# Optimization experiments

Hardware: AMD Instinct MI355X
Metric: run time of the kernel (lower is better)

## Reference

```python
import jax, jax.numpy as jnp
import numpy as np

N_NODES = 20000
N_RELS = 64
RP = 8
EMB = 64
N_CLASSES = 16
NT = 250000      # unique (subject, object) pairs
N_TRIPLES = 500000


def setup_inputs() -> dict:
    rng = np.random.default_rng(0)
    # sample candidate (s, o) pairs, dedupe (mirrors torch.unique(pairs, dim=0)),
    # keep exactly NT unique pairs
    cand = rng.integers(0, N_NODES, size=(NT + 60000, 2))
    pairs = np.unique(cand, axis=0)
    assert pairs.shape[0] >= NT
    pairs = pairs[:NT]
    # each triple maps to a unique-pair row and a relation column;
    # relation_matrix is the coalesced sparse_coo (nt, num_rels) densified
    row = rng.integers(0, NT, size=N_TRIPLES)
    rel = rng.integers(0, N_RELS, size=N_TRIPLES)
    relation_matrix = np.zeros((NT, N_RELS), dtype=np.float32)
    np.add.at(relation_matrix, (row, rel), 1.0)
    # hindices / vindices exactly as in __init__ (note the literal o*r / s*r):
    s, o = pairs[:, 0].astype(np.int64), pairs[:, 1].astype(np.int64)
    rm = np.arange(RP, dtype=np.int64)[:, None]
    hrow = np.tile(s, RP)                      # (RP*NT,) row in [0, N)
    hcol = (o[None, :] * rm).reshape(-1)       # (RP*NT,) col in [0, N*RP)
    vrow = (s[None, :] * rm).reshape(-1)       # (RP*NT,) row in [0, N*RP)
    vcol = np.tile(o, RP)                      # (RP*NT,) col in [0, N)

    key = jax.random.key(0)
    ks = jax.random.split(key, 6)

    def xavier(k, shape, fan_in, fan_out):
        gain = np.float32(np.sqrt(2.0))  # calculate_gain('relu')
        bound = gain * np.float32(np.sqrt(6.0 / (fan_in + fan_out)))
        return jax.random.uniform(k, shape, jnp.float32, -bound, bound)

    lb = np.float32(1.0 / np.sqrt(N_RELS))  # nn.Linear default init bound
    return {
        "relation_matrix": jnp.asarray(relation_matrix),
        "hrow": jnp.asarray(hrow), "hcol": jnp.asarray(hcol),
        "vrow": jnp.asarray(vrow), "vcol": jnp.asarray(vcol),
        "W_l1": jax.random.uniform(ks[0], (N_RELS, RP), jnp.float32, -lb, lb),
        "b_l1": jax.random.uniform(ks[1], (RP,), jnp.float32, -lb, lb),
        "W_l2": jax.random.uniform(ks[2], (N_RELS, RP), jnp.float32, -lb, lb),
        "b_l2": jax.random.uniform(ks[3], (RP,), jnp.float32, -lb, lb),
        "weights1": xavier(ks[4], (RP, N_NODES, EMB), N_NODES * EMB, RP * EMB),
        "weights2": xavier(ks[5], (RP, EMB, N_CLASSES), EMB * N_CLASSES, RP * N_CLASSES),
        "bias1": jnp.zeros((EMB,), jnp.float32),
        "bias2": jnp.zeros((N_CLASSES,), jnp.float32),
    }


def reference(relation_matrix, hrow, hcol, vrow, vcol,
              W_l1, b_l1, W_l2, b_l2, weights1, weights2, bias1, bias2):
    n, rp, e = N_NODES, RP, EMB
    nrp = n * rp
    # ---- hop 1: latent coefficients (to_latent1, ldepth=0 => single Linear)
    l1 = relation_matrix @ W_l1 + b_l1              # (NT, RP)
    l1 = l1.T.reshape(-1)                           # (RP*NT,) r-major, matches h/v index order
    # sum_sparse(hindices, l1, (n, n*rp), row=False): per-edge column-sum normalization
    colsum = jax.ops.segment_sum(l1, hcol, num_segments=nrp)
    l1 = l1 / colsum[hcol]
    # spmm over hindices: out[hrow] += l1 * weights1.view(n*rp, e)[hcol]
    Wflat = weights1.reshape(nrp, e)                # (N*RP, EMB)
    h = jax.ops.segment_sum(l1[:, None] * Wflat[hcol], hrow, num_segments=n)
    h = jax.nn.relu(h + bias1)                      # (N, EMB)
    # ---- hop 2
    l2 = jax.nn.softmax(relation_matrix @ W_l2 + b_l2, axis=1)  # (NT, RP)
    l2 = jax.nn.relu(l2.T.reshape(-1))              # (RP*NT,)
    # sum_sparse(vindices, l2, (n*rp, n), row=True): per-edge row-sum normalization
    rowsum = jax.ops.segment_sum(l2, vrow, num_segments=nrp)
    l2 = l2 / jnp.maximum(rowsum[vrow], 1e-6)
    # spmm over vindices: out[vrow] += l2 * h[vcol]
    h2 = jax.ops.segment_sum(l2[:, None] * h[vcol], vrow, num_segments=nrp)
    h2 = h2.reshape(rp, n, e)                       # (RP, N, EMB)
    logits = jnp.einsum('rhc,rnh->nc', weights2, h2) + bias2  # (N, C)
    return logits
```

## Files before the change

### kernel.cpp

```cpp
#include <hip/hip_runtime.h>
#include <hip/hip_fp16.h>

#define NT      250000
#define NN      20000
#define RP      8
#define EMB     64
#define NCLS    16
#define NRELS   64
#define REDB    64
#define KMAX    140000
#define GEMVB   977
#define RPB     79
#define HIB     977
#define OIB     1250

__global__ __launch_bounds__(256) void k_gemv(
    const float* __restrict__ rm,
    const float* __restrict__ W1, const float* __restrict__ b1,
    const float* __restrict__ W2, const float* __restrict__ b2,
    float* __restrict__ l1, float* __restrict__ l2,
    const int* __restrict__ hrow, int* __restrict__ rowptr,
    const int* __restrict__ vcol, int* __restrict__ cnt,
    float* __restrict__ out, const float* __restrict__ bias2)
{
    __shared__ float tile[256 * 20];
    int bid = blockIdx.x;
    if (bid >= GEMVB) {
        int b = bid - GEMVB;
        if (b < RPB) {
            int i = b * 256 + threadIdx.x;
            if (i > NN) return;
            int lo = 0, hi = NT;
            while (lo < hi) { int mid = (lo + hi) >> 1; if (hrow[mid] < i) lo = mid + 1; else hi = mid; }
            rowptr[i] = lo;
        } else if (b < RPB + HIB) {
            int p = (b - RPB) * 256 + threadIdx.x;
            if (p < NT) atomicAdd(&cnt[vcol[p]], 1);
        } else {
            int i = (b - RPB - HIB) * 256 + threadIdx.x;
            if (i < NN * NCLS) out[i] = bias2[i & (NCLS - 1)];
        }
        return;
    }
    int t = threadIdx.x;
    int base = bid * 256;
    float a1[8], a2[8];
#pragma unroll
    for (int r = 0; r < 8; ++r) { a1[r] = b1[r]; a2[r] = b2[r]; }

#pragma unroll 1
    for (int kc = 0; kc < 4; ++kc) {
        __syncthreads();
#pragma unroll
        for (int q = 0; q < 4; ++q) {
            int i = q * 256 + t;
            int pl = i >> 2, j4 = i & 3;
            int p = base + pl;
            float4 v = make_float4(0.f, 0.f, 0.f, 0.f);
            if (p < NT) v = reinterpret_cast<const float4*>(rm)[(size_t)p * 16 + kc * 4 + j4];
            *reinterpret_cast<float4*>(&tile[pl * 20 + j4 * 4]) = v;
        }
        __syncthreads();
        float xr[16];
#pragma unroll
        for (int j4 = 0; j4 < 4; ++j4) {
            float4 v = *reinterpret_cast<const float4*>(&tile[t * 20 + j4 * 4]);
            xr[j4 * 4 + 0] = v.x; xr[j4 * 4 + 1] = v.y;
            xr[j4 * 4 + 2] = v.z; xr[j4 * 4 + 3] = v.w;
        }
#pragma unroll
        for (int kk = 0; kk < 16; ++kk) {
            float x = xr[kk];
            int k = kc * 16 + kk;
#pragma unroll
            for (int r = 0; r < 8; ++r) {
                a1[r] = fmaf(x, W1[k * 8 + r], a1[r]);
                a2[r] = fmaf(x, W2[k * 8 + r], a2[r]);
            }
        }
    }
    int p = base + t;
    if (p >= NT) return;
    float mx = a2[0];
#pragma unroll
    for (int r = 1; r < 8; ++r) mx = fmaxf(mx, a2[r]);
    float sm = 0.f;
#pragma unroll
    for (int r = 0; r < 8; ++r) { a2[r] = __expf(a2[r] - mx); sm += a2[r]; }
    float inv = 1.0f / sm;
#pragma unroll
    for (int r = 0; r < 8; ++r) a2[r] *= inv;
    float4* o1 = reinterpret_cast<float4*>(l1 + (size_t)p * 8);
    float4* o2 = reinterpret_cast<float4*>(l2 + (size_t)p * 8);
    o1[0] = make_float4(a1[0], a1[1], a1[2], a1[3]);
    o1[1] = make_float4(a1[4], a1[5], a1[6], a1[7]);
    o2[0] = make_float4(a2[0], a2[1], a2[2], a2[3]);
    o2[1] = make_float4(a2[4], a2[5], a2[6], a2[7]);
}

__global__ __launch_bounds__(1024) void k_scan(
    const int* __restrict__ cnt, int* __restrict__ cstart, int* __restrict__ cnt2)
{
    __shared__ int part[1024];
    int t = threadIdx.x;
    int base = t * 20;
    int local[20];
    int s = 0;
#pragma unroll
    for (int i = 0; i < 20; ++i) {
        int idx = base + i;
        int c = (idx < NN) ? cnt[idx] : 0;
        local[i] = s;
        s += c;
    }
    part[t] = s;
    __syncthreads();
    for (int off = 1; off < 1024; off <<= 1) {
        int v = (t >= off) ? part[t - off] : 0;
        __syncthreads();
        part[t] += v;
        __syncthreads();
    }
    int ebase = t ? part[t - 1] : 0;
#pragma unroll
    for (int i = 0; i < 20; ++i) {
        int idx = base + i;
        if (idx < NN) { cstart[idx] = ebase + local[i]; cnt2[idx] = ebase + local[i]; }
    }
    if (t == 1023) cstart[NN] = part[1023];
}

__global__ __launch_bounds__(256) void k_pos(
    const int* __restrict__ vcol, int* __restrict__ cnt2, int* __restrict__ cscidx)
{
    int p = blockIdx.x * blockDim.x + threadIdx.x;
    if (p >= NT) return;
    int o = vcol[p];
    int slot = atomicAdd(&cnt2[o], 1);
    cscidx[slot] = p;
}

__global__ __launch_bounds__(256) void k_colsum(
    const float* __restrict__ l1, const int* __restrict__ cstart,
    const int* __restrict__ cscidx, float* __restrict__ colsum)
{
    int bid = blockIdx.x;
    if (bid < NN / 4) {
        int o = bid * 4 + (threadIdx.x >> 6);
        int lane = threadIdx.x & 63;
        int qb = cstart[o], qe = cstart[o + 1];
        if (qb == qe) return;
        int j = lane >> 3, r = lane & 7;
        float sum = 0.f;
        for (int q0 = qb; q0 < qe; q0 += 8) {
            int q = q0 + j;
            if (q < qe) sum += l1[(size_t)cscidx[q] * 8 + r];
        }
        sum += __shfl_xor(sum, 8, 64);
        sum += __shfl_xor(sum, 16, 64);
        sum += __shfl_xor(sum, 32, 64);
        if (lane >= 1 && lane < 8) atomicAdd(&colsum[o * lane], sum);
    } else {
        int b2 = bid - NN / 4;
        float s = 0.f;
        for (int i = b2 * 256 + threadIdx.x; i < NT; i += REDB * 256) s += l1[(size_t)i * 8];
        __shared__ float red[256];
        red[threadIdx.x] = s;
        __syncthreads();
        for (int off = 128; off > 0; off >>= 1) {
            if (threadIdx.x < off) red[threadIdx.x] += red[threadIdx.x + off];
            __syncthreads();
        }
        if (threadIdx.x == 0) atomicAdd(&colsum[0], red[0]);
    }
}

__global__ __launch_bounds__(256) void k_contrib(
    const float* __restrict__ l1, const float* __restrict__ colsum,
    const int* __restrict__ cstart, const int* __restrict__ cscidx,
    const float* __restrict__ w1, __half* __restrict__ contrib)
{
    int o = (int)((blockIdx.x * blockDim.x + threadIdx.x) >> 6);
    int lane = threadIdx.x & 63;
    if (o >= NN) return;
    int qb = cstart[o], qe = cstart[o + 1];
    if (qb == qe) return;
    float y[8];
    y[0] = w1[lane] / colsum[0];
#pragma unroll
    for (int r = 1; r < 8; ++r) {
        int seg = o * r;
        y[r] = w1[(size_t)seg * EMB + lane] / colsum[seg];
    }
    int q = qb;
    for (; q + 3 < qe; q += 4) {
        int p0 = cscidx[q], p1 = cscidx[q + 1], p2 = cscidx[q + 2], p3 = cscidx[q + 3];
        const float4* a4 = reinterpret_cast<const float4*>(l1 + (size_t)p0 * 8);
        const float4* b4 = reinterpret_cast<const float4*>(l1 + (size_t)p1 * 8);
        const float4* c4 = reinterpret_cast<const float4*>(l1 + (size_t)p2 * 8);
        const float4* d4 = reinterpret_cast<const float4*>(l1 + (size_t)p3 * 8);
        float4 A = a4[0], B = a4[1], C = b4[0], D = b4[1];
        float4 E = c4[0], F = c4[1], G = d4[0], H = d4[1];
        float v0 = A.x * y[0];
        v0 = fmaf(A.y, y[1], v0); v0 = fmaf(A.z, y[2], v0); v0 = fmaf(A.w, y[3], v0);
        v0 = fmaf(B.x, y[4], v0); v0 = fmaf(B.y, y[5], v0);
        v0 = fmaf(B.z, y[6], v0); v0 = fmaf(B.w, y[7], v0);
        float v1 = C.x * y[0];
        v1 = fmaf(C.y, y[1], v1); v1 = fmaf(C.z, y[2], v1); v1 = fmaf(C.w, y[3], v1);
        v1 = fmaf(D.x, y[4], v1); v1 = fmaf(D.y, y[5], v1);
        v1 = fmaf(D.z, y[6], v1); v1 = fmaf(D.w, y[7], v1);
        float v2 = E.x * y[0];
        v2 = fmaf(E.y, y[1], v2); v2 = fmaf(E.z, y[2], v2); v2 = fmaf(E.w, y[3], v2);
        v2 = fmaf(F.x, y[4], v2); v2 = fmaf(F.y, y[5], v2);
        v2 = fmaf(F.z, y[6], v2); v2 = fmaf(F.w, y[7], v2);
        float v3 = G.x * y[0];
        v3 = fmaf(G.y, y[1], v3); v3 = fmaf(G.z, y[2], v3); v3 = fmaf(G.w, y[3], v3);
        v3 = fmaf(H.x, y[4], v3); v3 = fmaf(H.y, y[5], v3);
        v3 = fmaf(H.z, y[6], v3); v3 = fmaf(H.w, y[7], v3);
        contrib[(size_t)p0 * EMB + lane] = __float2half(v0);
        contrib[(size_t)p1 * EMB + lane] = __float2half(v1);
        contrib[(size_t)p2 * EMB + lane] = __float2half(v2);
        contrib[(size_t)p3 * EMB + lane] = __float2half(v3);
    }
    for (; q < qe; ++q) {
        int p0 = cscidx[q];
        const float4* a4 = reinterpret_cast<const float4*>(l1 + (size_t)p0 * 8);
        float4 A = a4[0], B = a4[1];
        float v0 = A.x * y[0];
        v0 = fmaf(A.y, y[1], v0); v0 = fmaf(A.z, y[2], v0); v0 = fmaf(A.w, y[3], v0);
        v0 = fmaf(B.x, y[4], v0); v0 = fmaf(B.y, y[5], v0);
        v0 = fmaf(B.z, y[6], v0); v0 = fmaf(B.w, y[7], v0);
        contrib[(size_t)p0 * EMB + lane] = __float2half(v0);
    }
}

__global__ __launch_bounds__(256) void k_h(
    const __half* __restrict__ contrib, const float* __restrict__ l2,
    const int* __restrict__ rowptr, const float* __restrict__ bias1,
    __half* __restrict__ h, float* __restrict__ rowsum, float* __restrict__ rs0part)
{
    int s = (int)((blockIdx.x * blockDim.x + threadIdx.x) >> 6);
    int lane = threadIdx.x & 63;
    if (s >= NN) return;
    int pb = rowptr[s], pe = rowptr[s + 1];
    float acc = 0.f;
    for (int p = pb; p < pe; ++p)
        acc += __half2float(contrib[(size_t)p * EMB + lane]);
    h[(size_t)s * EMB + lane] = __float2half(fmaxf(acc + bias1[lane], 0.f));

    float psum = 0.f;
    for (int p0 = pb + (lane >> 3); p0 < pe; p0 += 8)
        psum += l2[(size_t)p0 * 8 + (lane & 7)];
    psum += __shfl_xor(psum, 8, 64);
    psum += __shfl_xor(psum, 16, 64);
    psum += __shfl_xor(psum, 32, 64);
    if (s == 0) {
        float tt = psum;
        tt += __shfl_xor(tt, 1, 64);
        tt += __shfl_xor(tt, 2, 64);
        tt += __shfl_xor(tt, 4, 64);
        if (lane == 0) rs0part[0] = tt;
    } else {
        if (lane == 0) rs0part[s] = psum;
        else if (lane < 8) atomicAdd(&rowsum[s * lane], psum);
    }
}

__global__ __launch_bounds__(256) void k_l2out(
    const float* __restrict__ l2, const int* __restrict__ rowptr,
    const int* __restrict__ vcol, const __half* __restrict__ h,
    const float* __restrict__ rowsum, const float* __restrict__ w2,
    float* __restrict__ out, float* __restrict__ Abuf0)
{
    int s = (int)((blockIdx.x * blockDim.x + threadIdx.x) >> 6);
    int lane = threadIdx.x & 63;
    if (s >= NN) return;
    int pb = rowptr[s], pe = rowptr[s + 1];
    float sc[8];
#pragma unroll
    for (int rr = 1; rr < 8; ++rr)
        sc[rr] = (s > 0) ? (1.0f / fmaxf(rowsum[s * rr], 1e-6f)) : 0.f;
    float acc[8];
#pragma unroll
    for (int r = 0; r < 8; ++r) acc[r] = 0.f;
    int p = pb;
    for (; p + 3 < pe; p += 4) {
        int o0 = vcol[p], o1 = vcol[p + 1], o2 = vcol[p + 2], o3 = vcol[p + 3];
        float hv0 = __half2float(h[(size_t)o0 * EMB + lane]);
        float hv1 = __half2float(h[(size_t)o1 * EMB + lane]);
        float hv2 = __half2float(h[(size_t)o2 * EMB + lane]);
        float hv3 = __half2float(h[(size_t)o3 * EMB + lane]);
        const float4* q4 = reinterpret_cast<const float4*>(l2 + (size_t)p * 8);
        float4 A = q4[0], B = q4[1], C = q4[2], D = q4[3];
        float4 E = q4[4], F = q4[5], G = q4[6], H = q4[7];
        acc[0] = fmaf(A.x, hv0, fmaf(C.x, hv1, fmaf(E.x, hv2, fmaf(G.x, hv3, acc[0]))));
        acc[1] = fmaf(A.y, hv0, fmaf(C.y, hv1, fmaf(E.y, hv2, fmaf(G.y, hv3, acc[1]))));
        acc[2] = fmaf(A.z, hv0, fmaf(C.z, hv1, fmaf(E.z, hv2, fmaf(G.z, hv3, acc[2]))));
        acc[3] = fmaf(A.w, hv0, fmaf(C.w, hv1, fmaf(E.w, hv2, fmaf(G.w, hv3, acc[3]))));
        acc[4] = fmaf(B.x, hv0, fmaf(D.x, hv1, fmaf(F.x, hv2, fmaf(H.x, hv3, acc[4]))));
        acc[5] = fmaf(B.y, hv0, fmaf(D.y, hv1, fmaf(F.y, hv2, fmaf(H.y, hv3, acc[5]))));
        acc[6] = fmaf(B.z, hv0, fmaf(D.z, hv1, fmaf(F.z, hv2, fmaf(H.z, hv3, acc[6]))));
        acc[7] = fmaf(B.w, hv0, fmaf(D.w, hv1, fmaf(F.w, hv2, fmaf(H.w, hv3, acc[7]))));
    }
    for (; p < pe; ++p) {
        int o0 = vcol[p];
        float hv0 = __half2float(h[(size_t)o0 * EMB + lane]);
        const float4* q4 = reinterpret_cast<const float4*>(l2 + (size_t)p * 8);
        float4 A = q4[0], B = q4[1];
        acc[0] = fmaf(A.x, hv0, acc[0]); acc[1] = fmaf(A.y, hv0, acc[1]);
        acc[2] = fmaf(A.z, hv0, acc[2]); acc[3] = fmaf(A.w, hv0, acc[3]);
        acc[4] = fmaf(B.x, hv0, acc[4]); acc[5] = fmaf(B.y, hv0, acc[5]);
        acc[6] = fmaf(B.z, hv0, acc[6]); acc[7] = fmaf(B.w, hv0, acc[7]);
    }
    if (s == 0) {
        float a = acc[0] + acc[1] + acc[2] + acc[3] +
                  acc[4] + acc[5] + acc[6] + acc[7];
        Abuf0[lane] = a;
        return;
    }
    Abuf0[(size_t)s * EMB + lane] = acc[0];
    if (pb == pe) return;
    int hq = lane >> 4, c = lane & 15;
#pragma unroll
    for (int rr = 1; rr < 8; ++rr) {
        int k = s * rr;
        int rp = k / NN;
        int n  = k - rp * NN;
        float v = 0.f;
#pragma unroll
        for (int hh = 0; hh < 16; ++hh) {
            float av = __shfl(acc[rr], hq * 16 + hh, 64);
            v = fmaf(av, w2[((rp * EMB) + (hq * 16 + hh)) * NCLS + c], v);
        }
        v += __shfl_xor(v, 16, 64);
        v += __shfl_xor(v, 32, 64);
        if (lane < 16) atomicAdd(&out[(size_t)n * NCLS + lane], v * sc[rr]);
    }
}

__global__ __launch_bounds__(256) void k_redA(
    const float* __restrict__ Abuf0, const float* __restrict__ rs0part,
    const float* __restrict__ w2, float* __restrict__ out)
{
    __shared__ float red[256];
    __shared__ float part[64];
    __shared__ float irs0s;
    float sv = 0.f;
    for (int i = threadIdx.x; i < NN; i += 256) sv += rs0part[i];
    red[threadIdx.x] = sv;
    __syncthreads();
    for (int off = 128; off > 0; off >>= 1) {
        if (threadIdx.x < off) red[threadIdx.x] += red[threadIdx.x + off];
        __syncthreads();
    }
    if (threadIdx.x == 0) irs0s = 1.0f / fmaxf(red[0], 1e-6f);
    __syncthreads();
    float irs0 = irs0s;
    int lane = threadIdx.x & 63, w = threadIdx.x >> 6;
    float sum = 0.f;
    for (int ss = blockIdx.x + 64 * w; ss < NN; ss += 256)
        sum += Abuf0[(size_t)ss * EMB + lane];
    red[threadIdx.x] = sum;
    __syncthreads();
    if (threadIdx.x < 64) {
        part[threadIdx.x] = red[threadIdx.x] + red[threadIdx.x + 64] +
                            red[threadIdx.x + 128] + red[threadIdx.x + 192];
    }
    __syncthreads();
    if (threadIdx.x < 64) {
        int hq = threadIdx.x >> 4, c = threadIdx.x & 15;
        float v = 0.f;
#pragma unroll
        for (int hh = 0; hh < 16; ++hh) {
            int hd = hq * 16 + hh;
            v = fmaf(part[hd], w2[hd * NCLS + c], v);
        }
        v += __shfl_xor(v, 16, 64);
        v += __shfl_xor(v, 32, 64);
        if (threadIdx.x < 16) atomicAdd(&out[c], v * irs0);
    }
}

extern "C" void kernel_launch(void* const* d_in, const int* in_sizes, int n_in,
                              void* d_out, int out_size, void* d_ws, size_t ws_size,
                              hipStream_t stream)
{
    const float* rm    = (const float*)d_in[0];
    const int*   hrow  = (const int*)d_in[1];
    const int*   vcol  = (const int*)d_in[4];
    const float* W1    = (const float*)d_in[5];
    const float* b1    = (const float*)d_in[6];
    const float* W2    = (const float*)d_in[7];
    const float* b2    = (const float*)d_in[8];
    const float* w1    = (const float*)d_in[9];
    const float* w2    = (const float*)d_in[10];
    const float* bias1 = (const float*)d_in[11];
    const float* bias2 = (const float*)d_in[12];
    float* out = (float*)d_out;

    float* ws = (float*)d_ws;
    float*  l1      = ws;
    float*  l2      = ws + 2000000;
    int*    rowptr  = (int*)(ws + 4000000);
    float*  colsum  = ws + 4100000;
    float*  rowsum  = ws + 4260000;
    __half* h       = (__half*)(ws + 4400000);
    int*    cnt     = (int*)(ws + 5040000);
    int*    cstart  = cnt + 20000;
    int*    cnt2    = cstart + 20001;
    int*    cscidx  = cnt2 + 20000;
    __half* contrib = (__half*)(ws + 5600000);
    float*  Abuf0   = ws;
    float*  rs0part = ws + 1280000;

    hipMemsetAsync(colsum, 0, (size_t)300000 * sizeof(float), stream);
    hipMemsetAsync(cnt, 0, (size_t)20000 * sizeof(int), stream);

    k_gemv   <<<GEMVB + RPB + HIB + OIB, 256, 0, stream>>>(rm, W1, b1, W2, b2, l1, l2,
                                                           hrow, rowptr, vcol, cnt, out, bias2);
    k_scan   <<<1, 1024, 0, stream>>>(cnt, cstart, cnt2);
    k_pos    <<<(NT + 255) / 256, 256, 0, stream>>>(vcol, cnt2, cscidx);
    k_colsum <<<NN / 4 + REDB, 256, 0, stream>>>(l1, cstart, cscidx, colsum);
    k_contrib<<<(NN * 64) / 256, 256, 0, stream>>>(l1, colsum, cstart, cscidx, w1, contrib);
    k_h      <<<(NN * 64) / 256, 256, 0, stream>>>(contrib, l2, rowptr, bias1, h, rowsum, rs0part);
    k_l2out  <<<(NN * 64) / 256, 256, 0, stream>>>(l2, rowptr, vcol, h, rowsum, w2, out, Abuf0);
    k_redA   <<<64, 256, 0, stream>>>(Abuf0, rs0part, w2, out);
}
```

Baseline: 233.2 us.

## Scatter hop-1 contributions via float atomics instead of half staging buffer

The per-pair contribution kernel now atomically adds each fp32 value straight into a per-subject accumulator h_acc. Previously it wrote a 250000x64 half buffer that k_h then re-read and summed per row. This removes a large intermediate write and read pass but adds 16M global float atomics, which may contend on popular subjects and make summation order nondeterministic. The workspace is rearranged so a single memset zeroes cnt, colsum, rowsum and h_acc. A reciprocal division is also swapped for the hardware rcp intrinsic.

After: 255.4 us. 1.09x slower.

```diff
diff --git a/kernel.cpp b/kernel.cpp
--- a/kernel.cpp
+++ b/kernel.cpp
@@ -175,10 +175,11 @@
     }
 }
 
-__global__ __launch_bounds__(256) void k_contrib(
+__global__ __launch_bounds__(256) void k_hacc(
     const float* __restrict__ l1, const float* __restrict__ colsum,
     const int* __restrict__ cstart, const int* __restrict__ cscidx,
-    const float* __restrict__ w1, __half* __restrict__ contrib)
+    const int* __restrict__ hrow, const float* __restrict__ w1,
+    float* __restrict__ h_acc)
 {
     int o = (int)((blockIdx.x * blockDim.x + threadIdx.x) >> 6);
     int lane = threadIdx.x & 63;
@@ -195,6 +196,7 @@
     int q = qb;
     for (; q + 3 < qe; q += 4) {
         int p0 = cscidx[q], p1 = cscidx[q + 1], p2 = cscidx[q + 2], p3 = cscidx[q + 3];
+        int s0 = hrow[p0], s1 = hrow[p1], s2 = hrow[p2], s3 = hrow[p3];
         const float4* a4 = reinterpret_cast<const float4*>(l1 + (size_t)p0 * 8);
         const float4* b4 = reinterpret_cast<const float4*>(l1 + (size_t)p1 * 8);
         const float4* c4 = reinterpret_cast<const float4*>(l1 + (size_t)p2 * 8);
@@ -217,25 +219,26 @@
         v3 = fmaf(G.y, y[1], v3); v3 = fmaf(G.z, y[2], v3); v3 = fmaf(G.w, y[3], v3);
         v3 = fmaf(H.x, y[4], v3); v3 = fmaf(H.y, y[5], v3);
         v3 = fmaf(H.z, y[6], v3); v3 = fmaf(H.w, y[7], v3);
-        contrib[(size_t)p0 * EMB + lane] = __float2half(v0);
-        contrib[(size_t)p1 * EMB + lane] = __float2half(v1);
-        contrib[(size_t)p2 * EMB + lane] = __float2half(v2);
-        contrib[(size_t)p3 * EMB + lane] = __float2half(v3);
+        atomicAdd(&h_acc[(size_t)s0 * EMB + lane], v0);
+        atomicAdd(&h_acc[(size_t)s1 * EMB + lane], v1);
+        atomicAdd(&h_acc[(size_t)s2 * EMB + lane], v2);
+        atomicAdd(&h_acc[(size_t)s3 * EMB + lane], v3);
     }
     for (; q < qe; ++q) {
         int p0 = cscidx[q];
+        int s0 = hrow[p0];
         const float4* a4 = reinterpret_cast<const float4*>(l1 + (size_t)p0 * 8);
         float4 A = a4[0], B = a4[1];
         float v0 = A.x * y[0];
         v0 = fmaf(A.y, y[1], v0); v0 = fmaf(A.z, y[2], v0); v0 = fmaf(A.w, y[3], v0);
         v0 = fmaf(B.x, y[4], v0); v0 = fmaf(B.y, y[5], v0);
         v0 = fmaf(B.z, y[6], v0); v0 = fmaf(B.w, y[7], v0);
-        contrib[(size_t)p0 * EMB + lane] = __float2half(v0);
+        atomicAdd(&h_acc[(size_t)s0 * EMB + lane], v0);
     }
 }
 
 __global__ __launch_bounds__(256) void k_h(
-    const __half* __restrict__ contrib, const float* __restrict__ l2,
+    const float* __restrict__ h_acc, const float* __restrict__ l2,
     const int* __restrict__ rowptr, const float* __restrict__ bias1,
     __half* __restrict__ h, float* __restrict__ rowsum, float* __restrict__ rs0part)
 {
@@ -243,9 +246,7 @@
     int lane = threadIdx.x & 63;
     if (s >= NN) return;
     int pb = rowptr[s], pe = rowptr[s + 1];
-    float acc = 0.f;
-    for (int p = pb; p < pe; ++p)
-        acc += __half2float(contrib[(size_t)p * EMB + lane]);
+    float acc = h_acc[(size_t)s * EMB + lane];
     h[(size_t)s * EMB + lane] = __float2half(fmaxf(acc + bias1[lane], 0.f));
 
     float psum = 0.f;
@@ -279,7 +280,7 @@
     float sc[8];
 #pragma unroll
     for (int rr = 1; rr < 8; ++rr)
-        sc[rr] = (s > 0) ? (1.0f / fmaxf(rowsum[s * rr], 1e-6f)) : 0.f;
+        sc[rr] = (s > 0) ? __builtin_amdgcn_rcpf(fmaxf(rowsum[s * rr], 1e-6f)) : 0.f;
     float acc[8];
 #pragma unroll
     for (int r = 0; r < 8; ++r) acc[r] = 0.f;
@@ -402,27 +403,26 @@
     float*  l1      = ws;
     float*  l2      = ws + 2000000;
     int*    rowptr  = (int*)(ws + 4000000);
+    int*    cnt     = (int*)(ws + 4030000);
     float*  colsum  = ws + 4100000;
     float*  rowsum  = ws + 4260000;
-    __half* h       = (__half*)(ws + 4400000);
-    int*    cnt     = (int*)(ws + 5040000);
-    int*    cstart  = cnt + 20000;
+    float*  h_acc   = ws + 4400000;
+    __half* h       = (__half*)(ws + 5680000);
+    int*    cstart  = (int*)(ws + 6400000);
     int*    cnt2    = cstart + 20001;
     int*    cscidx  = cnt2 + 20000;
-    __half* contrib = (__half*)(ws + 5600000);
     float*  Abuf0   = ws;
     float*  rs0part = ws + 1280000;
 
-    hipMemsetAsync(colsum, 0, (size_t)300000 * sizeof(float), stream);
-    hipMemsetAsync(cnt, 0, (size_t)20000 * sizeof(int), stream);
+    hipMemsetAsync(cnt, 0, (size_t)(5680000 - 4030000) * sizeof(float), stream);
 
     k_gemv   <<<GEMVB + RPB + HIB + OIB, 256, 0, stream>>>(rm, W1, b1, W2, b2, l1, l2,
                                                            hrow, rowptr, vcol, cnt, out, bias2);
     k_scan   <<<1, 1024, 0, stream>>>(cnt, cstart, cnt2);
     k_pos    <<<(NT + 255) / 256, 256, 0, stream>>>(vcol, cnt2, cscidx);
     k_colsum <<<NN / 4 + REDB, 256, 0, stream>>>(l1, cstart, cscidx, colsum);
-    k_contrib<<<(NN * 64) / 256, 256, 0, stream>>>(l1, colsum, cstart, cscidx, w1, contrib);
-    k_h      <<<(NN * 64) / 256, 256, 0, stream>>>(contrib, l2, rowptr, bias1, h, rowsum, rs0part);
+    k_hacc   <<<(NN * 64) / 256, 256, 0, stream>>>(l1, colsum, cstart, cscidx, hrow, w1, h_acc);
+    k_h      <<<(NN * 64) / 256, 256, 0, stream>>>(h_acc, l2, rowptr, bias1, h, rowsum, rs0part);
     k_l2out  <<<(NN * 64) / 256, 256, 0, stream>>>(l2, rowptr, vcol, h, rowsum, w2, out, Abuf0);
     k_redA   <<<64, 256, 0, stream>>>(Abuf0, rs0part, w2, out);
 }
```
